# Optimization experiments

Hardware: AMD Instinct MI355X
Metric: run time of the kernel (lower is better)

Reference implementation:

```python
import jax, jax.numpy as jnp
from jax import lax
import numpy as np

B, T, F_IN, H = 64, 128, 12, 128  # batch, seq_len, input/output features, hidden


def _uinit(key, shape, fan):
    return jax.random.uniform(key, shape, jnp.float32, -1.0, 1.0) / np.float32(np.sqrt(fan))


def setup_inputs() -> dict:
    key = jax.random.key(0)
    ks = jax.random.split(key, 12)
    inp = {
        "x": jax.random.normal(ks[0], (B, T, F_IN), jnp.float32),
        # encoder LSTM (gate order i,f,g,o; b = b_ih + b_hh folded together)
        "enc_Wih": _uinit(ks[1], (4 * H, F_IN), H),
        "enc_Whh": _uinit(ks[2], (4 * H, H), H),
        "enc_b": _uinit(ks[3], (4 * H,), H),
        # decoder LSTM (input is the 12-dim teacher-forced x slice)
        "dec_Wih": _uinit(ks[4], (4 * H, F_IN), H),
        "dec_Whh": _uinit(ks[5], (4 * H, H), H),
        "dec_b": _uinit(ks[6], (4 * H,), H),
        # attention: Linear(2H -> H) with bias, then v: Linear(H -> 1, no bias)
        "attn_W": _uinit(ks[7], (H, 2 * H), 2 * H),
        "attn_b": _uinit(ks[8], (H,), 2 * H),
        "v_w": _uinit(ks[9], (H,), H),
        # output layer: Linear(2H -> F_IN)  (intended width; see notes)
        "out_W": _uinit(ks[10], (F_IN, 2 * H), 2 * H),
        "out_b": _uinit(ks[11], (F_IN,), 2 * H),
    }
    return inp


def _lstm_cell(xt, h, c, Wih, Whh, b):
    z = xt @ Wih.T + h @ Whh.T + b  # [B, 4H]
    i, f, g, o = jnp.split(z, 4, axis=-1)
    c = jax.nn.sigmoid(f) * c + jax.nn.sigmoid(i) * jnp.tanh(g)
    h = jax.nn.sigmoid(o) * jnp.tanh(c)
    return h, c


def reference(x, enc_Wih, enc_Whh, enc_b, dec_Wih, dec_Whh, dec_b,
              attn_W, attn_b, v_w, out_W, out_b):
    b_, t_, _ = x.shape
    hdim = enc_Whh.shape[1]
    xs = jnp.swapaxes(x, 0, 1)  # [T, B, F]
    h0 = jnp.zeros((b_, hdim), x.dtype)
    c0 = jnp.zeros((b_, hdim), x.dtype)

    def enc_step(carry, xt):
        h, c = carry
        h, c = _lstm_cell(xt, h, c, enc_Wih, enc_Whh, enc_b)
        return (h, c), h

    (hT, cT), enc_hs = lax.scan(enc_step, (h0, c0), xs)
    enc_out = jnp.swapaxes(enc_hs, 0, 1)  # [B, T, H]

    # split attn weight: cat(hidden, enc_out) @ W.T == hidden@W1.T + enc_out@W2.T
    W1, W2 = attn_W[:, :hdim], attn_W[:, hdim:]
    enc_proj = jnp.einsum("bth,gh->btg", enc_out, W2)  # precompute encoder side

    def dec_step(carry, xt):
        h, c = carry
        h, c = _lstm_cell(xt, h, c, dec_Wih, dec_Whh, dec_b)
        energy = jnp.tanh((h @ W1.T)[:, None, :] + enc_proj + attn_b)  # [B,T,H]
        score = jnp.einsum("bth,h->bt", energy, v_w)
        w = jax.nn.softmax(score, axis=1)  # attention over encoder time
        ctx = jnp.einsum("bt,bth->bh", w, enc_out)
        return (h, c), jnp.concatenate([h, ctx], axis=-1)  # [B, 2H]

    _, dec_ys = lax.scan(dec_step, (hT, cT), xs)
    dec_out = jnp.swapaxes(dec_ys, 0, 1)  # [B, T, 2H]
    return dec_out @ out_W.T + out_b  # [B, T, F]
```

## Files before the change

kernel.cpp:

```cpp
#include <hip/hip_runtime.h>
#include <hip/hip_bf16.h>

#define BB 64
#define TT 128
#define FIN 12
#define HH 128

#define LOG2E 1.4426950408889634f
#define TWO_LOG2E 2.8853900817779268f

__device__ __forceinline__ float fexp2(float x) { return __builtin_amdgcn_exp2f(x); }
__device__ __forceinline__ float frcp(float x)  { return __builtin_amdgcn_rcpf(x); }

__device__ __forceinline__ float tanh_f(float x) {
  return 1.0f - 2.0f * frcp(1.0f + fexp2(TWO_LOG2E * x));
}
__device__ __forceinline__ float sigm_f(float x) {
  return frcp(1.0f + fexp2(-LOG2E * x));
}

template <int CTRL>
__device__ __forceinline__ float dpp_addstage(float v) {
  int s = __builtin_amdgcn_update_dpp(0, __float_as_int(v), CTRL, 0xF, 0xF, true);
  return v + __int_as_float(s);
}
__device__ __forceinline__ float red8(float v) {
  v = dpp_addstage<0xB1>(v);
  v = dpp_addstage<0x4E>(v);
  v = dpp_addstage<0x141>(v);
  return v;
}

#define FMA4S(acc, s, v) do { \
  acc.x = fmaf((s), (v).x, acc.x); \
  acc.y = fmaf((s), (v).y, acc.y); \
  acc.z = fmaf((s), (v).z, acc.z); \
  acc.w = fmaf((s), (v).w, acc.w); } while (0)

#define ACC4(hv, wv, a) do { \
  a = fmaf((hv).x, (wv).x, a); a = fmaf((hv).y, (wv).y, a); \
  a = fmaf((hv).z, (wv).z, a); a = fmaf((hv).w, (wv).w, a); } while (0)

__device__ __forceinline__ void lstm_phase(
    const float* __restrict__ Wih, const float* __restrict__ Whh,
    const float* __restrict__ bias, float* __restrict__ Hout ,
    float* __restrict__ xs, float (*hbuf)[160], float* __restrict__ hist,
    const int tid, const int q, const int i, float& c)
{
  const int xo   = (q < 4) ? 3 * q : 0;
  const float xz = (q < 4) ? 1.0f : 0.0f;

  float4 wg[4][4];
  #pragma unroll
  for (int g = 0; g < 4; ++g)
    #pragma unroll
    for (int j = 0; j < 4; ++j)
      wg[g][j] = *(const float4*)(Whh + ((g * HH + i) * HH) + 16 * q + 4 * j);

  float wx[4][3];
  #pragma unroll
  for (int g = 0; g < 4; ++g)
    #pragma unroll
    for (int j = 0; j < 3; ++j)
      wx[g][j] = Wih[(g * HH + i) * FIN + xo + j] * xz;

  const float bi = bias[i], bf = bias[HH + i], bg = bias[2 * HH + i], bo = bias[3 * HH + i];

  int ts = 0;
  #pragma unroll 1
  for (int half = 0; half < 2; ++half) {
    #pragma unroll 1
    for (int tt = 0; tt < 64; ++tt, ++ts) {
      const int t = half * 64 + tt;
      __syncthreads();
      const float* hb = (const float*)hbuf[ts & 1] + q * 20;
      float4 h0 = *(const float4*)(hb + 0);
      float4 h1 = *(const float4*)(hb + 4);
      float4 h2 = *(const float4*)(hb + 8);
      float4 h3 = *(const float4*)(hb + 12);

      const float* xt = xs + t * FIN + xo;
      float x0 = xt[0], x1 = xt[1], x2 = xt[2];
      float ai = wx[0][0] * x0 + wx[0][1] * x1 + wx[0][2] * x2;
      float af = wx[1][0] * x0 + wx[1][1] * x1 + wx[1][2] * x2;
      float ag = wx[2][0] * x0 + wx[2][1] * x1 + wx[2][2] * x2;
      float ao = wx[3][0] * x0 + wx[3][1] * x1 + wx[3][2] * x2;

      ACC4(h0, wg[0][0], ai); ACC4(h0, wg[1][0], af); ACC4(h0, wg[2][0], ag); ACC4(h0, wg[3][0], ao);
      ACC4(h1, wg[0][1], ai); ACC4(h1, wg[1][1], af); ACC4(h1, wg[2][1], ag); ACC4(h1, wg[3][1], ao);
      ACC4(h2, wg[0][2], ai); ACC4(h2, wg[1][2], af); ACC4(h2, wg[2][2], ag); ACC4(h2, wg[3][2], ao);
      ACC4(h3, wg[0][3], ai); ACC4(h3, wg[1][3], af); ACC4(h3, wg[2][3], ag); ACC4(h3, wg[3][3], ao);

      ai = red8(ai); af = red8(af); ag = red8(ag); ao = red8(ao);

      if (q == 0) {
        float zi = sigm_f(ai + bi);
        float zf = sigm_f(af + bf);
        float zg = tanh_f(ag + bg);
        float zo = sigm_f(ao + bo);
        c = fmaf(zf, c, zi * zg);
        float hn = zo * tanh_f(c);
        hbuf[(ts + 1) & 1][(i >> 4) * 20 + (i & 15)] = hn;
        hist[tt * HH + i] = hn;
      }
    }
    __syncthreads();
    {
      float4* dst = (float4*)(Hout + (size_t)(half * 64) * HH);
      const float4* src = (const float4*)hist;
      dst[tid]        = src[tid];
      dst[tid + 1024] = src[tid + 1024];
    }
  }
}

__global__ __launch_bounds__(1024, 4) void lstm_enc_kernel(
    const float* __restrict__ x,
    const float* __restrict__ eWih, const float* __restrict__ eWhh, const float* __restrict__ eb,
    float* __restrict__ encH, float* __restrict__ decH)
{
  const int b   = blockIdx.x;
  const int tid = threadIdx.x;
  const int q   = tid & 7;
  const int i   = tid >> 3;

  __shared__ __align__(16) float xs[TT * FIN];
  __shared__ __align__(16) float hbuf[2][160];
  __shared__ __align__(16) float hist[64 * HH];

  if (tid < (TT * FIN / 4))
    ((float4*)xs)[tid] = ((const float4*)(x + (size_t)b * TT * FIN))[tid];
  if (tid < 320) ((float*)hbuf)[tid] = 0.0f;
  float c = 0.0f;

  lstm_phase(eWih, eWhh, eb, encH + (size_t)b * TT * HH, xs, hbuf, hist, tid, q, i, c);

  if (q == 0) decH[(size_t)b * TT * HH + i] = c;
}

__global__ __launch_bounds__(1024, 4) void lstm_dec_p_kernel(
    const float* __restrict__ x,
    const float* __restrict__ dWih, const float* __restrict__ dWhh, const float* __restrict__ db,
    const float* __restrict__ attnW, const float* __restrict__ outW,
    const float* __restrict__ encH,
    float* __restrict__ decH, float* __restrict__ Pbuf, float* __restrict__ y2buf)
{
  __shared__ __align__(16) float smem[12416];
  const int tid = threadIdx.x;

  if (blockIdx.x < 64) {
    const int b = blockIdx.x;
    const int q = tid & 7;
    const int i = tid >> 3;
    float* xs           = smem;
    float (*hbuf)[160]  = (float(*)[160])(smem + 1536);
    float* hist         = smem + 1856;

    if (tid < (TT * FIN / 4))
      ((float4*)xs)[tid] = ((const float4*)(x + (size_t)b * TT * FIN))[tid];
    if (tid < 128) {
      float hv = encH[((size_t)b * TT + 127) * HH + tid];
      hbuf[0][(tid >> 4) * 20 + (tid & 15)] = hv;
    }
    float c = 0.0f;
    if (q == 0) c = decH[(size_t)b * TT * HH + i];

    lstm_phase(dWih, dWhh, db, decH + (size_t)b * TT * HH, xs, hbuf, hist, tid, q, i, c);
  } else if (blockIdx.x < 192) {
    const int pb = blockIdx.x - 64;
    const int b  = pb & 63;
    const int r0 = (pb >> 6) * 64;
    float* WT = smem;
    float* Xt = smem + 4224;

    const float* X = encH + ((size_t)b * TT + r0) * HH;
    ((float4*)Xt)[tid]        = ((const float4*)X)[tid];
    ((float4*)Xt)[tid + 1024] = ((const float4*)X)[tid + 1024];

    const float* W = attnW + HH;
    const int hq = tid & 31, rr = tid >> 5;
    const int h0 = 4 * hq;

    float4 acc0 = make_float4(0.f, 0.f, 0.f, 0.f);
    float4 acc1 = acc0;

    #pragma unroll 1
    for (int kb = 0; kb < 4; ++kb) {
      __syncthreads();
      {
        int h = tid >> 3, koff = (tid & 7) * 4;
        float4 v = *(const float4*)(W + h * 256 + kb * 32 + koff);
        WT[(koff + 0) * 132 + h] = v.x;
        WT[(koff + 1) * 132 + h] = v.y;
        WT[(koff + 2) * 132 + h] = v.z;
        WT[(koff + 3) * 132 + h] = v.w;
      }
      __syncthreads();
      const float* xr0 = Xt + (2 * rr) * 128 + kb * 32;
      const float* xr1 = xr0 + 128;
      #pragma unroll
      for (int k4 = 0; k4 < 32; k4 += 4) {
        float4 xa = *(const float4*)(xr0 + k4);
        float4 xb = *(const float4*)(xr1 + k4);
        float4 w0 = *(const float4*)&WT[(k4 + 0) * 132 + h0];
        float4 w1 = *(const float4*)&WT[(k4 + 1) * 132 + h0];
        float4 w2 = *(const float4*)&WT[(k4 + 2) * 132 + h0];
        float4 w3 = *(const float4*)&WT[(k4 + 3) * 132 + h0];
        FMA4S(acc0, xa.x, w0); FMA4S(acc0, xa.y, w1);
        FMA4S(acc0, xa.z, w2); FMA4S(acc0, xa.w, w3);
        FMA4S(acc1, xb.x, w0); FMA4S(acc1, xb.y, w1);
        FMA4S(acc1, xb.z, w2); FMA4S(acc1, xb.w, w3);
      }
    }
    acc0.x = fexp2(TWO_LOG2E * acc0.x); acc0.y = fexp2(TWO_LOG2E * acc0.y);
    acc0.z = fexp2(TWO_LOG2E * acc0.z); acc0.w = fexp2(TWO_LOG2E * acc0.w);
    acc1.x = fexp2(TWO_LOG2E * acc1.x); acc1.y = fexp2(TWO_LOG2E * acc1.y);
    acc1.z = fexp2(TWO_LOG2E * acc1.z); acc1.w = fexp2(TWO_LOG2E * acc1.w);
    float* O = Pbuf + ((size_t)b * TT + r0) * HH;
    *(float4*)(O + (2 * rr) * 128 + h0)     = acc0;
    *(float4*)(O + (2 * rr + 1) * 128 + h0) = acc1;
  } else if (y2buf) {
    const int b = blockIdx.x - 192;
    float* w2l = smem;
    if (tid < 384) {
      int f = tid >> 5, k = (tid & 31) * 4;
      float4 wv = *(const float4*)(outW + f * 256 + 128 + k);
      *(float4*)&w2l[f * 132 + k] = wv;
    }
    __syncthreads();
    for (int j = tid; j < TT * 12; j += 1024) {
      int t = j / 12, f = j - 12 * t;
      const float* er = encH + ((size_t)b * TT + t) * HH;
      const float* wr = w2l + f * 132;
      float a = 0.f;
      #pragma unroll 8
      for (int k = 0; k < 32; ++k) {
        float4 ev = *(const float4*)(er + 4 * k);
        float4 wv = *(const float4*)(wr + 4 * k);
        ACC4(ev, wv, a);
      }
      y2buf[b * (TT * 16) + t * 16 + f] = a;
    }
  }
}

__global__ __launch_bounds__(256, 2) void projA_kernel(
    const float* __restrict__ decH, const float* __restrict__ attnW,
    const float* __restrict__ attnb, float* __restrict__ Abuf)
{
  const int b  = blockIdx.x & 63;
  const int r0 = (blockIdx.x >> 6) * 16;
  const int tid = threadIdx.x;

  __shared__ __align__(16) float WT[64 * 128];
  __shared__ __align__(16) float Xt[16 * 128];

  const float* X = decH + ((size_t)b * TT + r0) * HH;
  const float* W = attnW;

  ((float4*)Xt)[tid]       = ((const float4*)X)[tid];
  ((float4*)Xt)[256 + tid] = ((const float4*)X)[256 + tid];

  const int hq = tid & 31, rr = tid >> 5;
  const int h0 = 4 * hq;

  float4 acc0 = *(const float4*)(attnb + h0);
  float4 acc1 = acc0;

  for (int kb = 0; kb < 2; ++kb) {
    __syncthreads();
    {
      int h = tid >> 1, koff = (tid & 1) * 32;
      #pragma unroll
      for (int j = 0; j < 8; ++j) {
        float4 v = *(const float4*)(W + h * 256 + kb * 64 + koff + 4 * j);
        int kp = koff + 4 * j;
        WT[(kp + 0) * 128 + h] = v.x;
        WT[(kp + 1) * 128 + h] = v.y;
        WT[(kp + 2) * 128 + h] = v.z;
        WT[(kp + 3) * 128 + h] = v.w;
      }
    }
    __syncthreads();
    const float* xr0 = Xt + (2 * rr) * 128 + kb * 64;
    const float* xr1 = xr0 + 128;
    #pragma unroll
    for (int k4 = 0; k4 < 64; k4 += 4) {
      float4 xa = *(const float4*)(xr0 + k4);
      float4 xb = *(const float4*)(xr1 + k4);
      float4 w0 = *(const float4*)&WT[(k4 + 0) * 128 + h0];
      float4 w1 = *(const float4*)&WT[(k4 + 1) * 128 + h0];
      float4 w2 = *(const float4*)&WT[(k4 + 2) * 128 + h0];
      float4 w3 = *(const float4*)&WT[(k4 + 3) * 128 + h0];
      FMA4S(acc0, xa.x, w0); FMA4S(acc0, xa.y, w1);
      FMA4S(acc0, xa.z, w2); FMA4S(acc0, xa.w, w3);
      FMA4S(acc1, xb.x, w0); FMA4S(acc1, xb.y, w1);
      FMA4S(acc1, xb.z, w2); FMA4S(acc1, xb.w, w3);
    }
  }
  acc0.x = fexp2(TWO_LOG2E * acc0.x); acc0.y = fexp2(TWO_LOG2E * acc0.y);
  acc0.z = fexp2(TWO_LOG2E * acc0.z); acc0.w = fexp2(TWO_LOG2E * acc0.w);
  acc1.x = fexp2(TWO_LOG2E * acc1.x); acc1.y = fexp2(TWO_LOG2E * acc1.y);
  acc1.z = fexp2(TWO_LOG2E * acc1.z); acc1.w = fexp2(TWO_LOG2E * acc1.w);
  float* O = Abuf + ((size_t)b * TT + r0) * HH;
  *(float4*)(O + (2 * rr) * 128 + h0)     = acc0;
  *(float4*)(O + (2 * rr + 1) * 128 + h0) = acc1;
}

#define AST 132
#define Y2ST 20

__global__ __launch_bounds__(512, 2) void attn_fused_kernel(
    const float* __restrict__ decH, const float* __restrict__ Pbuf,
    const float* __restrict__ y2buf,
    const float* __restrict__ attnW, const float* __restrict__ attnb,
    const float* __restrict__ vw, const float* __restrict__ outW,
    const float* __restrict__ outb, float* __restrict__ out)
{
  const int b  = blockIdx.x >> 2;
  const int s0 = (blockIdx.x & 3) * 32;
  const int tid = threadIdx.x;

  __shared__ __align__(16) float buf[64 * 128];
  __shared__ __align__(16) float a_lds[32 * AST];
  __shared__ __align__(16) float sc[32 * AST];
  __shared__ __align__(16) float dh[32 * 128];
  __shared__ __align__(16) float vl[HH];
  __shared__ __align__(16) float y2s[TT * Y2ST];

  ((float4*)dh)[tid]       = ((const float4*)(decH + ((size_t)b * TT + s0) * HH))[tid];
  ((float4*)dh)[tid + 512] = ((const float4*)(decH + ((size_t)b * TT + s0) * HH))[tid + 512];
  if (tid < 32) ((float4*)vl)[tid] = ((const float4*)vw)[tid];
  {
    float4 v = ((const float4*)(y2buf + (size_t)b * (TT * 16)))[tid];
    int t = tid >> 2, g = (tid & 3) * 4;
    *(float4*)&y2s[t * Y2ST + g] = v;
  }

  const int hq = tid & 31, rr = tid >> 5;
  const int h0 = 4 * hq;
  {
    float4 acc0 = *(const float4*)(attnb + h0);
    float4 acc1 = acc0;
    #pragma unroll 1
    for (int kb = 0; kb < 2; ++kb) {
      __syncthreads();
      {
        int h = tid >> 2, koff = (tid & 3) * 16;
        #pragma unroll
        for (int j = 0; j < 4; ++j) {
          float4 v = *(const float4*)(attnW + h * 256 + kb * 64 + koff + 4 * j);
          int kp = koff + 4 * j;
          buf[(kp + 0) * 128 + h] = v.x;
          buf[(kp + 1) * 128 + h] = v.y;
          buf[(kp + 2) * 128 + h] = v.z;
          buf[(kp + 3) * 128 + h] = v.w;
        }
      }
      __syncthreads();
      const float* xr0 = dh + (2 * rr) * 128 + kb * 64;
      const float* xr1 = xr0 + 128;
      #pragma unroll
      for (int k4 = 0; k4 < 64; k4 += 4) {
        float4 xa = *(const float4*)(xr0 + k4);
        float4 xb = *(const float4*)(xr1 + k4);
        float4 w0 = *(const float4*)&buf[(k4 + 0) * 128 + h0];
        float4 w1 = *(const float4*)&buf[(k4 + 1) * 128 + h0];
        float4 w2 = *(const float4*)&buf[(k4 + 2) * 128 + h0];
        float4 w3 = *(const float4*)&buf[(k4 + 3) * 128 + h0];
        FMA4S(acc0, xa.x, w0); FMA4S(acc0, xa.y, w1);
        FMA4S(acc0, xa.z, w2); FMA4S(acc0, xa.w, w3);
        FMA4S(acc1, xb.x, w0); FMA4S(acc1, xb.y, w1);
        FMA4S(acc1, xb.z, w2); FMA4S(acc1, xb.w, w3);
      }
    }
    acc0.x = fexp2(TWO_LOG2E * acc0.x); acc0.y = fexp2(TWO_LOG2E * acc0.y);
    acc0.z = fexp2(TWO_LOG2E * acc0.z); acc0.w = fexp2(TWO_LOG2E * acc0.w);
    acc1.x = fexp2(TWO_LOG2E * acc1.x); acc1.y = fexp2(TWO_LOG2E * acc1.y);
    acc1.z = fexp2(TWO_LOG2E * acc1.z); acc1.w = fexp2(TWO_LOG2E * acc1.w);
    *(float4*)&a_lds[(2 * rr) * AST + h0]     = acc0;
    *(float4*)&a_lds[(2 * rr + 1) * AST + h0] = acc1;
  }

  const int uq = tid & 15;
  const int sl = tid >> 4;

  float4 sA, sB;
  #pragma unroll 1
  for (int half = 0; half < 2; ++half) {
    __syncthreads();
    #pragma unroll
    for (int i = 0; i < 4; ++i) {
      int flat = i * 2048 + tid * 4;
      int tp = flat >> 7;
      int hh0 = flat & 127;
      float4 v = *(const float4*)(Pbuf + ((size_t)b * TT + half * 64 + tp) * HH + hh0);
      int tq = tp >> 2, tr = tp & 3;
      buf[(hh0 + 0) * 64 + 4 * ((tq ^ ((hh0 + 0) >> 2)) & 15) + tr] = v.x;
      buf[(hh0 + 1) * 64 + 4 * ((tq ^ ((hh0 + 1) >> 2)) & 15) + tr] = v.y;
      buf[(hh0 + 2) * 64 + 4 * ((tq ^ ((hh0 + 2) >> 2)) & 15) + tr] = v.z;
      buf[(hh0 + 3) * 64 + 4 * ((tq ^ ((hh0 + 3) >> 2)) & 15) + tr] = v.w;
    }
    __syncthreads();
    float4 acc = make_float4(0.f, 0.f, 0.f, 0.f);
    const float* earow = a_lds + sl * AST;
    #pragma unroll 4
    for (int h = 0; h < 128; h += 4) {
      float4 ea = *(const float4*)&earow[h];
      float4 va = *(const float4*)&vl[h];
      const int xoff = 4 * ((uq ^ ((h >> 2) & 15)) & 15);
      float4 p0 = *(const float4*)&buf[(h + 0) * 64 + xoff];
      float4 p1 = *(const float4*)&buf[(h + 1) * 64 + xoff];
      float4 p2 = *(const float4*)&buf[(h + 2) * 64 + xoff];
      float4 p3 = *(const float4*)&buf[(h + 3) * 64 + xoff];
      acc.x = fmaf(va.x, frcp(fmaf(ea.x, p0.x, 1.f)), acc.x);
      acc.y = fmaf(va.x, frcp(fmaf(ea.x, p0.y, 1.f)), acc.y);
      acc.z = fmaf(va.x, frcp(fmaf(ea.x, p0.z, 1.f)), acc.z);
      acc.w = fmaf(va.x, frcp(fmaf(ea.x, p0.w, 1.f)), acc.w);
      acc.x = fmaf(va.y, frcp(fmaf(ea.y, p1.x, 1.f)), acc.x);
      acc.y = fmaf(va.y, frcp(fmaf(ea.y, p1.y, 1.f)), acc.y);
      acc.z = fmaf(va.y, frcp(fmaf(ea.y, p1.z, 1.f)), acc.z);
      acc.w = fmaf(va.y, frcp(fmaf(ea.y, p1.w, 1.f)), acc.w);
      acc.x = fmaf(va.z, frcp(fmaf(ea.z, p2.x, 1.f)), acc.x);
      acc.y = fmaf(va.z, frcp(fmaf(ea.z, p2.y, 1.f)), acc.y);
      acc.z = fmaf(va.z, frcp(fmaf(ea.z, p2.z, 1.f)), acc.z);
      acc.w = fmaf(va.z, frcp(fmaf(ea.z, p2.w, 1.f)), acc.w);
      acc.x = fmaf(va.w, frcp(fmaf(ea.w, p3.x, 1.f)), acc.x);
      acc.y = fmaf(va.w, frcp(fmaf(ea.w, p3.y, 1.f)), acc.y);
      acc.z = fmaf(va.w, frcp(fmaf(ea.w, p3.z, 1.f)), acc.z);
      acc.w = fmaf(va.w, frcp(fmaf(ea.w, p3.w, 1.f)), acc.w);
    }
    float4 o;
    o.x = -2.f * acc.x; o.y = -2.f * acc.y;
    o.z = -2.f * acc.z; o.w = -2.f * acc.w;
    if (half == 0) sA = o; else sB = o;
  }

  {
    float mx = fmaxf(fmaxf(fmaxf(sA.x, sA.y), fmaxf(sA.z, sA.w)),
                     fmaxf(fmaxf(sB.x, sB.y), fmaxf(sB.z, sB.w)));
    #pragma unroll
    for (int msk = 1; msk <= 8; msk <<= 1) mx = fmaxf(mx, __shfl_xor(mx, msk, 64));
    float4 eA, eB;
    eA.x = fexp2(LOG2E * (sA.x - mx)); eA.y = fexp2(LOG2E * (sA.y - mx));
    eA.z = fexp2(LOG2E * (sA.z - mx)); eA.w = fexp2(LOG2E * (sA.w - mx));
    eB.x = fexp2(LOG2E * (sB.x - mx)); eB.y = fexp2(LOG2E * (sB.y - mx));
    eB.z = fexp2(LOG2E * (sB.z - mx)); eB.w = fexp2(LOG2E * (sB.w - mx));
    float sm = ((eA.x + eA.y) + (eA.z + eA.w)) + ((eB.x + eB.y) + (eB.z + eB.w));
    #pragma unroll
    for (int msk = 1; msk <= 8; msk <<= 1) sm += __shfl_xor(sm, msk, 64);
    float r = frcp(sm);
    eA.x *= r; eA.y *= r; eA.z *= r; eA.w *= r;
    eB.x *= r; eB.y *= r; eB.z *= r; eB.w *= r;
    *(float4*)&sc[sl * AST + 4 * uq]      = eA;
    *(float4*)&sc[sl * AST + 64 + 4 * uq] = eB;
  }
  __syncthreads();

  if (tid < 384) {
    int s = tid / 12, f = tid - 12 * (tid / 12);
    float acc = outb[f];
    const float4* w4 = (const float4*)(outW + f * 256);
    const float4* d4 = (const float4*)(dh + s * 128);
    #pragma unroll
    for (int k = 0; k < 32; ++k) {
      float4 wv = w4[k], dv = d4[k];
      acc = fmaf(wv.x, dv.x, acc); acc = fmaf(wv.y, dv.y, acc);
      acc = fmaf(wv.z, dv.z, acc); acc = fmaf(wv.w, dv.w, acc);
    }
    const float* wrow = sc + s * AST;
    #pragma unroll 8
    for (int t = 0; t < TT; ++t)
      acc = fmaf(wrow[t], y2s[t * Y2ST + f], acc);
    out[((size_t)b * TT + s0 + s) * FIN + f] = acc;
  }
}

__global__ __launch_bounds__(512, 2) void attn_kernel_fb(
    const float* __restrict__ encH, const float* __restrict__ decH,
    const float* __restrict__ Pbuf, const float* __restrict__ Abuf,
    const float* __restrict__ vw, const float* __restrict__ outW,
    const float* __restrict__ outb, float* __restrict__ out)
{
  const int b  = blockIdx.x >> 3;
  const int s0 = (blockIdx.x & 7) * 16;
  const int tid = threadIdx.x;

  __shared__ __align__(16) float buf[64 * 128];
  __shared__ __align__(16) float a_lds[16 * AST];
  __shared__ __align__(16) float sc[16 * AST];
  __shared__ __align__(16) float dh[16 * 128];
  __shared__ __align__(16) float vl[HH];
  __shared__ __align__(16) float y2s[TT * Y2ST];
  __shared__ __align__(16) float w2l[12 * AST];

  ((float4*)dh)[tid] = ((const float4*)(decH + ((size_t)b * TT + s0) * HH))[tid];
  if (tid < 32) ((float4*)vl)[tid] = ((const float4*)vw)[tid];
  {
    int r = tid >> 5, c4 = (tid & 31) * 4;
    float4 av = *(const float4*)(Abuf + ((size_t)b * TT + s0 + r) * HH + c4);
    *(float4*)&a_lds[r * AST + c4] = av;
  }
  if (tid < 384) {
    int f = tid >> 5, k = (tid & 31) * 4;
    float4 wv = *(const float4*)(outW + f * 256 + 128 + k);
    *(float4*)&w2l[f * AST + k] = wv;
  }

  const int u  = tid & 31;
  const int sl = tid >> 5;
  const int uq = u & 15;
  const int uh = u >> 4;

  for (int half = 0; half < 2; ++half) {
    const int tbase = half * 64;
    __syncthreads();
    #pragma unroll
    for (int i = 0; i < 4; ++i) {
      int flat = i * 2048 + tid * 4;
      int tp = flat >> 7;
      int h0 = flat & 127;
      float4 v = *(const float4*)(Pbuf + ((size_t)b * TT + tbase + tp) * HH + h0);
      int tq = tp >> 2, tr = tp & 3;
      buf[(h0 + 0) * 64 + 4 * ((tq ^ ((h0 + 0) >> 2)) & 15) + tr] = v.x;
      buf[(h0 + 1) * 64 + 4 * ((tq ^ ((h0 + 1) >> 2)) & 15) + tr] = v.y;
      buf[(h0 + 2) * 64 + 4 * ((tq ^ ((h0 + 2) >> 2)) & 15) + tr] = v.z;
      buf[(h0 + 3) * 64 + 4 * ((tq ^ ((h0 + 3) >> 2)) & 15) + tr] = v.w;
    }
    __syncthreads();
    float4 acc = make_float4(0.f, 0.f, 0.f, 0.f);
    const float* earow = a_lds + sl * AST;
    #pragma unroll 4
    for (int hh = 0; hh < 64; hh += 4) {
      const int h = uh * 64 + hh;
      float4 ea = *(const float4*)&earow[h];
      float4 va = *(const float4*)&vl[h];
      const int xoff = 4 * ((uq ^ ((h >> 2) & 15)) & 15);
      float4 p0 = *(const float4*)&buf[(h + 0) * 64 + xoff];
      float4 p1 = *(const float4*)&buf[(h + 1) * 64 + xoff];
      float4 p2 = *(const float4*)&buf[(h + 2) * 64 + xoff];
      float4 p3 = *(const float4*)&buf[(h + 3) * 64 + xoff];
      acc.x = fmaf(va.x, frcp(fmaf(ea.x, p0.x, 1.f)), acc.x);
      acc.y = fmaf(va.x, frcp(fmaf(ea.x, p0.y, 1.f)), acc.y);
      acc.z = fmaf(va.x, frcp(fmaf(ea.x, p0.z, 1.f)), acc.z);
      acc.w = fmaf(va.x, frcp(fmaf(ea.x, p0.w, 1.f)), acc.w);
      acc.x = fmaf(va.y, frcp(fmaf(ea.y, p1.x, 1.f)), acc.x);
      acc.y = fmaf(va.y, frcp(fmaf(ea.y, p1.y, 1.f)), acc.y);
      acc.z = fmaf(va.y, frcp(fmaf(ea.y, p1.z, 1.f)), acc.z);
      acc.w = fmaf(va.y, frcp(fmaf(ea.y, p1.w, 1.f)), acc.w);
      acc.x = fmaf(va.z, frcp(fmaf(ea.z, p2.x, 1.f)), acc.x);
      acc.y = fmaf(va.z, frcp(fmaf(ea.z, p2.y, 1.f)), acc.y);
      acc.z = fmaf(va.z, frcp(fmaf(ea.z, p2.z, 1.f)), acc.z);
      acc.w = fmaf(va.z, frcp(fmaf(ea.z, p2.w, 1.f)), acc.w);
      acc.x = fmaf(va.w, frcp(fmaf(ea.w, p3.x, 1.f)), acc.x);
      acc.y = fmaf(va.w, frcp(fmaf(ea.w, p3.y, 1.f)), acc.y);
      acc.z = fmaf(va.w, frcp(fmaf(ea.w, p3.z, 1.f)), acc.z);
      acc.w = fmaf(va.w, frcp(fmaf(ea.w, p3.w, 1.f)), acc.w);
    }
    acc.x += __shfl_xor(acc.x, 16, 64);
    acc.y += __shfl_xor(acc.y, 16, 64);
    acc.z += __shfl_xor(acc.z, 16, 64);
    acc.w += __shfl_xor(acc.w, 16, 64);
    if (uh == 0) {
      float4 o;
      o.x = -2.f * acc.x; o.y = -2.f * acc.y;
      o.z = -2.f * acc.z; o.w = -2.f * acc.w;
      *(float4*)&sc[sl * AST + tbase + 4 * uq] = o;
    }
  }
  __syncthreads();

  {
    float4 sv = *(const float4*)&sc[sl * AST + 4 * u];
    float mx = fmaxf(fmaxf(sv.x, sv.y), fmaxf(sv.z, sv.w));
    #pragma unroll
    for (int msk = 1; msk <= 16; msk <<= 1) mx = fmaxf(mx, __shfl_xor(mx, msk, 64));
    float4 e;
    e.x = fexp2(LOG2E * (sv.x - mx));
    e.y = fexp2(LOG2E * (sv.y - mx));
    e.z = fexp2(LOG2E * (sv.z - mx));
    e.w = fexp2(LOG2E * (sv.w - mx));
    float sm = (e.x + e.y) + (e.z + e.w);
    #pragma unroll
    for (int msk = 1; msk <= 16; msk <<= 1) sm += __shfl_xor(sm, msk, 64);
    float r = frcp(sm);
    e.x *= r; e.y *= r; e.z *= r; e.w *= r;
    *(float4*)&sc[sl * AST + 4 * u] = e;
  }

  for (int half = 0; half < 2; ++half) {
    const int tbase = half * 64;
    __syncthreads();
    #pragma unroll
    for (int i = 0; i < 4; ++i) {
      int flat = i * 2048 + tid * 4;
      int tp = flat >> 7;
      int hh0 = flat & 127;
      *(float4*)&buf[tp * 128 + hh0] =
          *(const float4*)(encH + ((size_t)b * TT + tbase + tp) * HH + hh0);
    }
    __syncthreads();
    {
      int j = tid;
      int t = j / 12, f = j - 12 * t;
      float a = 0.f;
      const float* br = buf + t * 128;
      const float* wr = w2l + f * AST;
      #pragma unroll 8
      for (int k = 0; k < 32; ++k) {
        float4 bv = *(const float4*)(br + 4 * k);
        float4 wv = *(const float4*)(wr + 4 * k);
        ACC4(bv, wv, a);
      }
      y2s[(tbase + t) * Y2ST + f] = a;
      if (tid < 256) {
        int j2 = tid + 512;
        int t2 = j2 / 12, f2 = j2 - 12 * t2;
        float a2 = 0.f;
        const float* br2 = buf + t2 * 128;
        const float* wr2 = w2l + f2 * AST;
        #pragma unroll 8
        for (int k = 0; k < 32; ++k) {
          float4 bv = *(const float4*)(br2 + 4 * k);
          float4 wv = *(const float4*)(wr2 + 4 * k);
          ACC4(bv, wv, a2);
        }
        y2s[(tbase + t2) * Y2ST + f2] = a2;
      }
    }
  }
  __syncthreads();

  if (tid < 192) {
    int s = tid / 12, f = tid - 12 * (tid / 12);
    float acc = outb[f];
    const float4* w4 = (const float4*)(outW + f * 256);
    const float4* d4 = (const float4*)(dh + s * 128);
    #pragma unroll
    for (int k = 0; k < 32; ++k) {
      float4 wv = w4[k], dv = d4[k];
      acc = fmaf(wv.x, dv.x, acc); acc = fmaf(wv.y, dv.y, acc);
      acc = fmaf(wv.z, dv.z, acc); acc = fmaf(wv.w, dv.w, acc);
    }
    const float* wrow = sc + s * AST;
    #pragma unroll 8
    for (int t = 0; t < TT; ++t)
      acc = fmaf(wrow[t], y2s[t * Y2ST + f], acc);
    out[((size_t)b * TT + s0 + s) * FIN + f] = acc;
  }
}

extern "C" void kernel_launch(void* const* d_in, const int* in_sizes, int n_in,
                              void* d_out, int out_size, void* d_ws, size_t ws_size,
                              hipStream_t stream)
{
  const float* x     = (const float*)d_in[0];
  const float* eWih  = (const float*)d_in[1];
  const float* eWhh  = (const float*)d_in[2];
  const float* eb    = (const float*)d_in[3];
  const float* dWih  = (const float*)d_in[4];
  const float* dWhh  = (const float*)d_in[5];
  const float* db    = (const float*)d_in[6];
  const float* attnW = (const float*)d_in[7];
  const float* attnb = (const float*)d_in[8];
  const float* vw    = (const float*)d_in[9];
  const float* outW  = (const float*)d_in[10];
  const float* outb  = (const float*)d_in[11];
  float* out = (float*)d_out;

  float* ws   = (float*)d_ws;
  const size_t SEG = (size_t)BB * TT * HH;
  float* encH = ws;
  float* decH = ws + SEG;
  float* Pbuf = ws + 2 * SEG;
  float* Abuf = ws + 3 * SEG;
  float* y2buf = ws + 4 * SEG;

  const size_t need_bytes = (4 * SEG + (size_t)BB * TT * 16) * sizeof(float);
  const bool have_y2 = ws_size >= need_bytes;

  lstm_enc_kernel<<<64, 1024, 0, stream>>>(x, eWih, eWhh, eb, encH, decH);
  if (have_y2) {
    lstm_dec_p_kernel<<<256, 1024, 0, stream>>>(x, dWih, dWhh, db, attnW, outW,
                                                encH, decH, Pbuf, y2buf);
    attn_fused_kernel<<<256, 512, 0, stream>>>(decH, Pbuf, y2buf, attnW, attnb,
                                               vw, outW, outb, out);
  } else {
    lstm_dec_p_kernel<<<192, 1024, 0, stream>>>(x, dWih, dWhh, db, attnW, outW,
                                                encH, decH, Pbuf, nullptr);
    projA_kernel<<<512, 256, 0, stream>>>(decH, attnW, attnb, Abuf);
    attn_kernel_fb<<<512, 512, 0, stream>>>(encH, decH, Pbuf, Abuf,
                                            vw, outW, outb, out);
  }
}
```

Baseline: 315.2 us.

## Use 1024-thread attention block staging all encoder timesteps in LDS at once

The fused attention kernel now launches 1024 threads per block instead of 512. The whole 128-step encoder projection for a batch is staged into a 128x128 shared buffer in one pass, replacing the previous two-half loop with its extra syncs and reloads. The attention weight transpose gets its own padded shared array, and the score/softmax phase now gives each thread one half of a row, reducing across 32 lanes. In exchange, shared memory use grows to nearly the full per-CU capacity, and half the threads sit idle during the small projection GEMM.

```diff
diff --git a/kernel.cpp b/kernel.cpp
--- a/kernel.cpp
+++ b/kernel.cpp
@@ -310,7 +310,7 @@
 #define AST 132
 #define Y2ST 20
 
-__global__ __launch_bounds__(512, 2) void attn_fused_kernel(
+__global__ __launch_bounds__(1024, 4) void attn_fused2_kernel(
     const float* __restrict__ decH, const float* __restrict__ Pbuf,
     const float* __restrict__ y2buf,
     const float* __restrict__ attnW, const float* __restrict__ attnb,
@@ -318,101 +318,105 @@
     const float* __restrict__ outb, float* __restrict__ out)
 {
   const int b  = blockIdx.x >> 2;
-  const int s0 = (blockIdx.x & 3) * 32;
+  const int s0 = (blockIdx.x & 2) * 16 + (blockIdx.x & 1) * 32 * 2;
+  const int s0p = (blockIdx.x & 3) * 32;
   const int tid = threadIdx.x;
 
-  __shared__ __align__(16) float buf[64 * 128];
+  __shared__ __align__(16) float buf[128 * 128];
+  __shared__ __align__(16) float w1t[64 * 132];
   __shared__ __align__(16) float a_lds[32 * AST];
   __shared__ __align__(16) float sc[32 * AST];
   __shared__ __align__(16) float dh[32 * 128];
+  __shared__ __align__(16) float y2s[TT * Y2ST];
   __shared__ __align__(16) float vl[HH];
-  __shared__ __align__(16) float y2s[TT * Y2ST];
-
-  ((float4*)dh)[tid]       = ((const float4*)(decH + ((size_t)b * TT + s0) * HH))[tid];
-  ((float4*)dh)[tid + 512] = ((const float4*)(decH + ((size_t)b * TT + s0) * HH))[tid + 512];
+
+  (void)s0;
+  ((float4*)dh)[tid] = ((const float4*)(decH + ((size_t)b * TT + s0p) * HH))[tid];
   if (tid < 32) ((float4*)vl)[tid] = ((const float4*)vw)[tid];
-  {
+  if (tid < 512) {
     float4 v = ((const float4*)(y2buf + (size_t)b * (TT * 16)))[tid];
     int t = tid >> 2, g = (tid & 3) * 4;
     *(float4*)&y2s[t * Y2ST + g] = v;
   }
-
-  const int hq = tid & 31, rr = tid >> 5;
-  const int h0 = 4 * hq;
+  #pragma unroll
+  for (int i = 0; i < 4; ++i) {
+    int flat = i * 4096 + tid * 4;
+    int tp = flat >> 7;
+    int h0f = flat & 127;
+    float4 v = *(const float4*)(Pbuf + ((size_t)b * TT + tp) * HH + h0f);
+    int hf = tp >> 6, tpl = tp & 63, tq = tpl >> 2, tr = tpl & 3;
+    int base = hf * 64 + tr;
+    buf[(h0f + 0) * 128 + base + 4 * ((tq ^ ((h0f + 0) >> 2)) & 15)] = v.x;
+    buf[(h0f + 1) * 128 + base + 4 * ((tq ^ ((h0f + 1) >> 2)) & 15)] = v.y;
+    buf[(h0f + 2) * 128 + base + 4 * ((tq ^ ((h0f + 2) >> 2)) & 15)] = v.z;
+    buf[(h0f + 3) * 128 + base + 4 * ((tq ^ ((h0f + 3) >> 2)) & 15)] = v.w;
+  }
+
   {
+    const int hq = tid & 31, rr = (tid >> 5) & 15;
+    const int h0 = 4 * hq;
     float4 acc0 = *(const float4*)(attnb + h0);
     float4 acc1 = acc0;
     #pragma unroll 1
     for (int kb = 0; kb < 2; ++kb) {
       __syncthreads();
       {
-        int h = tid >> 2, koff = (tid & 3) * 16;
+        int h = tid >> 3, koff = (tid & 7) * 8;
         #pragma unroll
-        for (int j = 0; j < 4; ++j) {
+        for (int j = 0; j < 2; ++j) {
           float4 v = *(const float4*)(attnW + h * 256 + kb * 64 + koff + 4 * j);
           int kp = koff + 4 * j;
-          buf[(kp + 0) * 128 + h] = v.x;
-          buf[(kp + 1) * 128 + h] = v.y;
-          buf[(kp + 2) * 128 + h] = v.z;
-          buf[(kp + 3) * 128 + h] = v.w;
+          w1t[(kp + 0) * 132 + h] = v.x;
+          w1t[(kp + 1) * 132 + h] = v.y;
+          w1t[(kp + 2) * 132 + h] = v.z;
+          w1t[(kp + 3) * 132 + h] = v.w;
         }
       }
       __syncthreads();
-      const float* xr0 = dh + (2 * rr) * 128 + kb * 64;
-      const float* xr1 = xr0 + 128;
-      #pragma unroll
-      for (int k4 = 0; k4 < 64; k4 += 4) {
-        float4 xa = *(const float4*)(xr0 + k4);
-        float4 xb = *(const float4*)(xr1 + k4);
-        float4 w0 = *(const float4*)&buf[(k4 + 0) * 128 + h0];
-        float4 w1 = *(const float4*)&buf[(k4 + 1) * 128 + h0];
-        float4 w2 = *(const float4*)&buf[(k4 + 2) * 128 + h0];
-        float4 w3 = *(const float4*)&buf[(k4 + 3) * 128 + h0];
-        FMA4S(acc0, xa.x, w0); FMA4S(acc0, xa.y, w1);
-        FMA4S(acc0, xa.z, w2); FMA4S(acc0, xa.w, w3);
-        FMA4S(acc1, xb.x, w0); FMA4S(acc1, xb.y, w1);
-        FMA4S(acc1, xb.z, w2); FMA4S(acc1, xb.w, w3);
-      }
-    }
-    acc0.x = fexp2(TWO_LOG2E * acc0.x); acc0.y = fexp2(TWO_LOG2E * acc0.y);
-    acc0.z = fexp2(TWO_LOG2E * acc0.z); acc0.w = fexp2(TWO_LOG2E * acc0.w);
-    acc1.x = fexp2(TWO_LOG2E * acc1.x); acc1.y = fexp2(TWO_LOG2E * acc1.y);
-    acc1.z = fexp2(TWO_LOG2E * acc1.z); acc1.w = fexp2(TWO_LOG2E * acc1.w);
-    *(float4*)&a_lds[(2 * rr) * AST + h0]     = acc0;
-    *(float4*)&a_lds[(2 * rr + 1) * AST + h0] = acc1;
-  }
-
-  const int uq = tid & 15;
-  const int sl = tid >> 4;
-
-  float4 sA, sB;
-  #pragma unroll 1
-  for (int half = 0; half < 2; ++half) {
-    __syncthreads();
-    #pragma unroll
-    for (int i = 0; i < 4; ++i) {
-      int flat = i * 2048 + tid * 4;
-      int tp = flat >> 7;
-      int hh0 = flat & 127;
-      float4 v = *(const float4*)(Pbuf + ((size_t)b * TT + half * 64 + tp) * HH + hh0);
-      int tq = tp >> 2, tr = tp & 3;
-      buf[(hh0 + 0) * 64 + 4 * ((tq ^ ((hh0 + 0) >> 2)) & 15) + tr] = v.x;
-      buf[(hh0 + 1) * 64 + 4 * ((tq ^ ((hh0 + 1) >> 2)) & 15) + tr] = v.y;
-      buf[(hh0 + 2) * 64 + 4 * ((tq ^ ((hh0 + 2) >> 2)) & 15) + tr] = v.z;
-      buf[(hh0 + 3) * 64 + 4 * ((tq ^ ((hh0 + 3) >> 2)) & 15) + tr] = v.w;
-    }
-    __syncthreads();
-    float4 acc = make_float4(0.f, 0.f, 0.f, 0.f);
-    const float* earow = a_lds + sl * AST;
+      if (tid < 512) {
+        const float* xr0 = dh + (2 * rr) * 128 + kb * 64;
+        const float* xr1 = xr0 + 128;
+        #pragma unroll
+        for (int k4 = 0; k4 < 64; k4 += 4) {
+          float4 xa = *(const float4*)(xr0 + k4);
+          float4 xb = *(const float4*)(xr1 + k4);
+          float4 w0 = *(const float4*)&w1t[(k4 + 0) * 132 + h0];
+          float4 w1 = *(const float4*)&w1t[(k4 + 1) * 132 + h0];
+          float4 w2 = *(const float4*)&w1t[(k4 + 2) * 132 + h0];
+          float4 w3 = *(const float4*)&w1t[(k4 + 3) * 132 + h0];
+          FMA4S(acc0, xa.x, w0); FMA4S(acc0, xa.y, w1);
+          FMA4S(acc0, xa.z, w2); FMA4S(acc0, xa.w, w3);
+          FMA4S(acc1, xb.x, w0); FMA4S(acc1, xb.y, w1);
+          FMA4S(acc1, xb.z, w2); FMA4S(acc1, xb.w, w3);
+        }
+      }
+    }
+    if (tid < 512) {
+      acc0.x = fexp2(TWO_LOG2E * acc0.x); acc0.y = fexp2(TWO_LOG2E * acc0.y);
+      acc0.z = fexp2(TWO_LOG2E * acc0.z); acc0.w = fexp2(TWO_LOG2E * acc0.w);
+      acc1.x = fexp2(TWO_LOG2E * acc1.x); acc1.y = fexp2(TWO_LOG2E * acc1.y);
+      acc1.z = fexp2(TWO_LOG2E * acc1.z); acc1.w = fexp2(TWO_LOG2E * acc1.w);
+      *(float4*)&a_lds[(2 * rr) * AST + h0]     = acc0;
+      *(float4*)&a_lds[(2 * rr + 1) * AST + h0] = acc1;
+    }
+  }
+  __syncthreads();
+
+  const int es  = tid >> 5;
+  const int ehf = (tid >> 4) & 1;
+  const int euq = tid & 15;
+  float4 acc = make_float4(0.f, 0.f, 0.f, 0.f);
+  {
+    const float* earow = a_lds + es * AST;
     #pragma unroll 4
     for (int h = 0; h < 128; h += 4) {
       float4 ea = *(const float4*)&earow[h];
       float4 va = *(const float4*)&vl[h];
-      const int xoff = 4 * ((uq ^ ((h >> 2) & 15)) & 15);
-      float4 p0 = *(const float4*)&buf[(h + 0) * 64 + xoff];
-      float4 p1 = *(const float4*)&buf[(h + 1) * 64 + xoff];
-      float4 p2 = *(const float4*)&buf[(h + 2) * 64 + xoff];
-      float4 p3 = *(const float4*)&buf[(h + 3) * 64 + xoff];
+      const int xoff = ehf * 64 + 4 * ((euq ^ ((h >> 2) & 15)) & 15);
+      float4 p0 = *(const float4*)&buf[(h + 0) * 128 + xoff];
+      float4 p1 = *(const float4*)&buf[(h + 1) * 128 + xoff];
+      float4 p2 = *(const float4*)&buf[(h + 2) * 128 + xoff];
+      float4 p3 = *(const float4*)&buf[(h + 3) * 128 + xoff];
       acc.x = fmaf(va.x, frcp(fmaf(ea.x, p0.x, 1.f)), acc.x);
       acc.y = fmaf(va.x, frcp(fmaf(ea.x, p0.y, 1.f)), acc.y);
       acc.z = fmaf(va.x, frcp(fmaf(ea.x, p0.z, 1.f)), acc.z);
@@ -430,49 +434,44 @@
       acc.z = fmaf(va.w, frcp(fmaf(ea.w, p3.z, 1.f)), acc.z);
       acc.w = fmaf(va.w, frcp(fmaf(ea.w, p3.w, 1.f)), acc.w);
     }
-    float4 o;
-    o.x = -2.f * acc.x; o.y = -2.f * acc.y;
-    o.z = -2.f * acc.z; o.w = -2.f * acc.w;
-    if (half == 0) sA = o; else sB = o;
+    acc.x = -2.f * acc.x; acc.y = -2.f * acc.y;
+    acc.z = -2.f * acc.z; acc.w = -2.f * acc.w;
   }
 
   {
-    float mx = fmaxf(fmaxf(fmaxf(sA.x, sA.y), fmaxf(sA.z, sA.w)),
-                     fmaxf(fmaxf(sB.x, sB.y), fmaxf(sB.z, sB.w)));
-    #pragma unroll
-    for (int msk = 1; msk <= 8; msk <<= 1) mx = fmaxf(mx, __shfl_xor(mx, msk, 64));
-    float4 eA, eB;
-    eA.x = fexp2(LOG2E * (sA.x - mx)); eA.y = fexp2(LOG2E * (sA.y - mx));
-    eA.z = fexp2(LOG2E * (sA.z - mx)); eA.w = fexp2(LOG2E * (sA.w - mx));
-    eB.x = fexp2(LOG2E * (sB.x - mx)); eB.y = fexp2(LOG2E * (sB.y - mx));
-    eB.z = fexp2(LOG2E * (sB.z - mx)); eB.w = fexp2(LOG2E * (sB.w - mx));
-    float sm = ((eA.x + eA.y) + (eA.z + eA.w)) + ((eB.x + eB.y) + (eB.z + eB.w));
-    #pragma unroll
-    for (int msk = 1; msk <= 8; msk <<= 1) sm += __shfl_xor(sm, msk, 64);
+    float mx = fmaxf(fmaxf(acc.x, acc.y), fmaxf(acc.z, acc.w));
+    #pragma unroll
+    for (int msk = 1; msk <= 16; msk <<= 1) mx = fmaxf(mx, __shfl_xor(mx, msk, 64));
+    float4 e;
+    e.x = fexp2(LOG2E * (acc.x - mx));
+    e.y = fexp2(LOG2E * (acc.y - mx));
+    e.z = fexp2(LOG2E * (acc.z - mx));
+    e.w = fexp2(LOG2E * (acc.w - mx));
+    float sm = (e.x + e.y) + (e.z + e.w);
+    #pragma unroll
+    for (int msk = 1; msk <= 16; msk <<= 1) sm += __shfl_xor(sm, msk, 64);
     float r = frcp(sm);
-    eA.x *= r; eA.y *= r; eA.z *= r; eA.w *= r;
-    eB.x *= r; eB.y *= r; eB.z *= r; eB.w *= r;
-    *(float4*)&sc[sl * AST + 4 * uq]      = eA;
-    *(float4*)&sc[sl * AST + 64 + 4 * uq] = eB;
+    e.x *= r; e.y *= r; e.z *= r; e.w *= r;
+    *(float4*)&sc[es * AST + ehf * 64 + 4 * euq] = e;
   }
   __syncthreads();
 
   if (tid < 384) {
     int s = tid / 12, f = tid - 12 * (tid / 12);
-    float acc = outb[f];
+    float acco = outb[f];
     const float4* w4 = (const float4*)(outW + f * 256);
     const float4* d4 = (const float4*)(dh + s * 128);
     #pragma unroll
     for (int k = 0; k < 32; ++k) {
       float4 wv = w4[k], dv = d4[k];
-      acc = fmaf(wv.x, dv.x, acc); acc = fmaf(wv.y, dv.y, acc);
-      acc = fmaf(wv.z, dv.z, acc); acc = fmaf(wv.w, dv.w, acc);
+      acco = fmaf(wv.x, dv.x, acco); acco = fmaf(wv.y, dv.y, acco);
+      acco = fmaf(wv.z, dv.z, acco); acco = fmaf(wv.w, dv.w, acco);
     }
     const float* wrow = sc + s * AST;
     #pragma unroll 8
     for (int t = 0; t < TT; ++t)
-      acc = fmaf(wrow[t], y2s[t * Y2ST + f], acc);
-    out[((size_t)b * TT + s0 + s) * FIN + f] = acc;
+      acco = fmaf(wrow[t], y2s[t * Y2ST + f], acco);
+    out[((size_t)b * TT + s0p + s) * FIN + f] = acco;
   }
 }
 
@@ -683,8 +682,8 @@
   if (have_y2) {
     lstm_dec_p_kernel<<<256, 1024, 0, stream>>>(x, dWih, dWhh, db, attnW, outW,
                                                 encH, decH, Pbuf, y2buf);
-    attn_fused_kernel<<<256, 512, 0, stream>>>(decH, Pbuf, y2buf, attnW, attnb,
-                                               vw, outW, outb, out);
+    attn_fused2_kernel<<<256, 1024, 0, stream>>>(decH, Pbuf, y2buf, attnW, attnb,
+                                                 vw, outW, outb, out);
   } else {
     lstm_dec_p_kernel<<<192, 1024, 0, stream>>>(x, dWih, dWhh, db, attnW, outW,
                                                 encH, decH, Pbuf, nullptr);
```

Measured after the change: 314.8 us. No clear change (-0.1%).
